# Performance work log

Measured on AMD Instinct MI355X. Metric: run time of the kernel, lower is better.

The kernel has to match this reference:

```python
import jax, jax.numpy as jnp
import numpy as np

H, W = 260, 346          # DAVIS346 sensor resolution
TEMP = 256.0             # time-decay temperature
B, T = 16, 4096          # batch, event sequence length
C = 2 * H + 2 * W        # pred channel dim = 1212


def setup_inputs() -> dict:
    key = jax.random.key(0)
    k1, k2, k3, k4, k5 = jax.random.split(key, 5)
    pred = jax.random.normal(k1, (B, T, C), dtype=jnp.float32)
    # target columns: [timestamp, y_index, x_index, polarity]
    t = jnp.sort(jax.random.uniform(k2, (B, T), minval=0.0, maxval=1.0e6), axis=1)
    y = jax.random.randint(k3, (B, T), 0, H)
    x = jax.random.randint(k4, (B, T), 0, W)
    p = jax.random.randint(k5, (B, T), 0, 2)
    target = jnp.stack([t,
                        y.astype(jnp.float32),
                        x.astype(jnp.float32),
                        p.astype(jnp.float32)], axis=-1)  # [B,T,4]
    return {"pred": pred, "target": target}


def _loss(pred, target):
    t = target[..., 0]                          # [B,T] timestamps
    y = target[..., 1].astype(jnp.int32)        # row indices
    x = target[..., 2].astype(jnp.int32)        # col indices
    p = target[..., 3]                          # polarity in {0,1}
    p_ = p[..., None]

    oh_y = jax.nn.one_hot(y, H, dtype=pred.dtype)   # [B,T,H]
    oh_x = jax.nn.one_hot(x, W, dtype=pred.dtype)   # [B,T,W]
    # scatter targets, concatenated in pred's channel layout [H0|H1|W0|W1]
    base = jnp.concatenate([oh_y * (1.0 - p_), oh_y * p_,
                            oh_x * (1.0 - p_), oh_x * p_], axis=-1)  # [B,T,C]

    # exponential time decay between consecutive events: d_i = exp(-(t_{i+1}-t_i)/TEMP)
    decay = jnp.exp(-(t[:, 1:] - t[:, :-1]) / TEMP)  # [B,T-1]

    # reverse recurrence: s_{T-1} = base_{T-1}; s_i = base_i + d_i * s_{i+1} for i = T-2..1;
    # s_0 = base_0 (torch loop stops before updating index 0)
    base_tm = jnp.swapaxes(base, 0, 1)               # [T,B,C] time-major
    decay_tm = jnp.swapaxes(decay, 0, 1)[..., None]  # [T-1,B,1]

    def step(carry, xd):
        b, d = xd
        s = b + d * carry
        return s, s

    _, ys = jax.lax.scan(step, base_tm[-1], (base_tm[:-1], decay_tm), reverse=True)
    s = jnp.concatenate([ys, base_tm[-1:]], axis=0)  # [T,B,C]
    s = s.at[0].set(base_tm[0])                      # index 0 never accumulated
    s = jnp.swapaxes(s, 0, 1)                        # [B,T,C]

    segs = [(0, H), (H, 2 * H), (2 * H, 2 * H + W), (2 * H + W, C)]
    losses = []
    for a, b in segs:
        logp = jax.nn.log_softmax(pred[..., a:b], axis=-1)
        soft = jax.nn.softmax(s[..., a:b], axis=-1)
        losses.append(-(soft * logp).sum(-1))        # soft-target CE, [B,T]
    lH0, lH1, lW0, lW1 = losses

    loss = ((lH0 + lW0) * (1.0 - p) + (lH1 + lW1) * p).mean()
    return loss


def reference(pred, target):
    return _loss(pred, target)
```

## Files before the change

kernel.cpp:

```cpp
#include <hip/hip_runtime.h>

#define HH 260
#define WW 346
#define CC 1212
#define CP 1280
#define HALF 640
#define NA 606
#define BB 16
#define TT 4096
#define INV_TEMP (1.0f/256.0f)
#define KCH 256
#define LCH 16
#define NG 16
#define GSZ 16
#define GLEN (GSZ * LCH)
#define NJ 10

__global__ __launch_bounds__(256) void p1_local(const float* __restrict__ target,
                                                float* __restrict__ Lbuf) {
    const int blk = blockIdx.x;
    const int b = blk >> 6;
    const int k0 = (blk & 63) << 2;
    const int tid = threadIdx.x;
    const int w = tid >> 6, lane = tid & 63;
    const int k = k0 + w;
    const int a = k * LCH;

    __shared__ float tg[4][LCH][4];
    __shared__ float tnextS[4];
    tg[tid >> 6][(tid >> 2) & 15][tid & 3] =
        target[((size_t)b * TT + k0 * LCH) * 4 + tid];
    if (tid < 4) {
        const int kk = k0 + tid;
        tnextS[tid] = (kk < KCH - 1) ? target[((size_t)b * TT + (kk + 1) * LCH) * 4] : 0.0f;
    }
    __syncthreads();

    float s0[NJ], s1[NJ];
#pragma unroll
    for (int j = 0; j < NJ; ++j) { s0[j] = 0.f; s1[j] = 0.f; }

    for (int li = LCH - 1; li >= 0; --li) {
        const int i = a + li;
        const float ti = tg[w][li][0];
        const float tn = (li == LCH - 1) ? tnextS[w] : tg[w][li + 1][0];
        const float d = (i >= TT - 1) ? 0.0f : __expf(-(tn - ti) * INV_TEMP);
        const int y = (int)tg[w][li][1], x = (int)tg[w][li][2], p = (int)tg[w][li][3];
        const int uy = y, ux = 260 + x;
        if (p == 0) {
#pragma unroll
            for (int j = 0; j < NJ; ++j) {
                const int u = lane + 64 * j;
                const float add = (u == uy ? 1.f : 0.f) + (u == ux ? 1.f : 0.f);
                s0[j] = fmaf(s0[j], d, add);
                s1[j] *= d;
            }
        } else {
#pragma unroll
            for (int j = 0; j < NJ; ++j) {
                const int u = lane + 64 * j;
                const float add = (u == uy ? 1.f : 0.f) + (u == ux ? 1.f : 0.f);
                s1[j] = fmaf(s1[j], d, add);
                s0[j] *= d;
            }
        }
    }
    float* __restrict__ out = Lbuf + (size_t)(b * KCH + k) * CP;
#pragma unroll
    for (int j = 0; j < NJ; ++j) {
        out[lane + 64 * j] = s0[j];
        out[HALF + lane + 64 * j] = s1[j];
    }
}

__global__ __launch_bounds__(256) void p2a(const float* __restrict__ target,
                                           const float* __restrict__ Lbuf,
                                           float* __restrict__ LCin,
                                           float* __restrict__ GroupL) {
    const int blk = blockIdx.x;
    const int ct = blk % 5;
    const int bg = blk / 5;
    const int b = bg >> 4, g = bg & 15;
    const int c = ct * 256 + threadIdx.x;

    float carry = 0.f;
#pragma unroll
    for (int kk = GSZ - 1; kk >= 0; --kk) {
        const int k = g * GSZ + kk;
        const size_t idx = ((size_t)(b * KCH + k)) * CP + c;
        LCin[idx] = carry;
        float P = 0.f;
        if (k < KCH - 1) {
            const float ta = target[((size_t)b * TT + k * LCH) * 4];
            const float te = target[((size_t)b * TT + (k + 1) * LCH) * 4];
            P = __expf(-(te - ta) * INV_TEMP);
        }
        carry = fmaf(P, carry, Lbuf[idx]);
    }
    GroupL[(size_t)bg * CP + c] = carry;
}

__global__ __launch_bounds__(256) void p2b(const float* __restrict__ target,
                                           const float* __restrict__ GroupL,
                                           float* __restrict__ SC) {
    const int blk = blockIdx.x;
    const int ct = blk % 5;
    const int b = blk / 5;
    const int c = ct * 256 + threadIdx.x;

    float Gv[NG], GP[NG];
#pragma unroll
    for (int g = 0; g < NG; ++g)
        Gv[g] = GroupL[((size_t)(b * NG + g)) * CP + c];
#pragma unroll
    for (int g = 0; g < NG; ++g) {
        if (g < NG - 1) {
            const float ta = target[((size_t)b * TT + g * GLEN) * 4];
            const float te = target[((size_t)b * TT + (g + 1) * GLEN) * 4];
            GP[g] = __expf(-(te - ta) * INV_TEMP);
        } else GP[g] = 0.f;
    }
    float carry = 0.f;
#pragma unroll
    for (int g = NG - 1; g >= 0; --g) {
        SC[((size_t)(b * NG + g)) * CP + c] = carry;
        carry = fmaf(GP[g], carry, Gv[g]);
    }
}

__global__ __launch_bounds__(256, 6) void p3_loss(const float* __restrict__ pred,
                                                  const float* __restrict__ target,
                                                  const float* __restrict__ LCin,
                                                  const float* __restrict__ SC,
                                                  double* __restrict__ partials) {
    const int blk = blockIdx.x;
    const int b = blk >> 6;
    const int k0 = (blk & 63) << 2;
    const int tid = threadIdx.x;
    const int w = tid >> 6, lane = tid & 63;
    const int k = k0 + w;
    const int g = k >> 4;
    const int a = k * LCH;

    __shared__ float tg[4][LCH][4];
    __shared__ float tnextS[4];
    tg[tid >> 6][(tid >> 2) & 15][tid & 3] =
        target[((size_t)b * TT + k0 * LCH) * 4 + tid];
    if (tid < 4) {
        const int kk = k0 + tid;
        tnextS[tid] = (kk < KCH - 1) ? target[((size_t)b * TT + (kk + 1) * LCH) * 4] : 0.0f;
    }
    __syncthreads();

    float Qk = 0.f;
    if (g < NG - 1) {
        const float tge = target[((size_t)b * TT + (g + 1) * GLEN) * 4];
        const float tk1 = target[((size_t)b * TT + (k + 1) * LCH) * 4];
        Qk = __expf(-(tge - tk1) * INV_TEMP);
    }

    const float* __restrict__ lc = LCin + (size_t)(b * KCH + k) * CP;
    const float* __restrict__ sc = SC + ((size_t)(b * NG + g)) * CP;
    float s0[NJ], s1[NJ];
#pragma unroll
    for (int j = 0; j < NJ; ++j) {
        const int u = lane + 64 * j;
        s0[j] = fmaf(Qk, sc[u], lc[u]);
        s1[j] = fmaf(Qk, sc[HALF + u], lc[HALF + u]);
    }

    float prA[NJ], prB[NJ];
    {
        const int p = (int)tg[w][LCH - 1][3];
        const float* __restrict__ prow = pred + ((size_t)b * TT + a + LCH - 1) * CC;
#pragma unroll
        for (int j = 0; j < NJ; ++j) {
            const int u = lane + 64 * j;
            const int c = (u < 260) ? p * HH + u : 2 * HH + p * WW + (u - 260);
            prA[j] = (u < NA) ? prow[c] : 0.0f;
        }
    }

    double lacc = 0.0;
    for (int li = LCH - 1; li >= 0; --li) {
        if (li > 0) {
            const int pn = (int)tg[w][li - 1][3];
            const float* __restrict__ prow = pred + ((size_t)b * TT + a + li - 1) * CC;
#pragma unroll
            for (int j = 0; j < NJ; ++j) {
                const int u = lane + 64 * j;
                const int c = (u < 260) ? pn * HH + u : 2 * HH + pn * WW + (u - 260);
                prB[j] = (u < NA) ? prow[c] : 0.0f;
            }
        }

        const int i = a + li;
        const float ti = tg[w][li][0];
        const float tn = (li == LCH - 1) ? tnextS[w] : tg[w][li + 1][0];
        const float d = (i == 0 || i >= TT - 1) ? 0.0f : __expf(-(tn - ti) * INV_TEMP);
        const int y = (int)tg[w][li][1], x = (int)tg[w][li][2], p = (int)tg[w][li][3];
        const int uy = y, ux = 260 + x;

        float zpy = 0.f, zsy = 0.f, dty = 0.f;
        float zpx = 0.f, zsx = 0.f, dtx = 0.f;

        auto stepActive = [&](float (&SA)[NJ], float (&SO)[NJ]) {
#pragma unroll
            for (int j = 0; j < NJ; ++j) {
                const int u = lane + 64 * j;
                const float add = (u == uy ? 1.f : 0.f) + (u == ux ? 1.f : 0.f);
                SA[j] = fmaf(SA[j], d, add);
                SO[j] *= d;
                float es = __expf(SA[j]);
                float ep = __expf(prA[j]);
                if (j == NJ - 1) {
                    const float m = (u < NA) ? 1.f : 0.f;
                    es *= m; ep *= m;
                }
                if (j < 4) {
                    zpy += ep; zsy += es; dty = fmaf(es, prA[j], dty);
                } else if (j == 4) {
                    const bool isY = (u < 260);
                    zpy += isY ? ep : 0.f;
                    zsy += isY ? es : 0.f;
                    dty = fmaf(isY ? es : 0.f, prA[j], dty);
                    zpx += isY ? 0.f : ep;
                    zsx += isY ? 0.f : es;
                    dtx = fmaf(isY ? 0.f : es, prA[j], dtx);
                } else {
                    zpx += ep; zsx += es; dtx = fmaf(es, prA[j], dtx);
                }
            }
        };
        if (p == 0) stepActive(s0, s1); else stepActive(s1, s0);

#pragma unroll
        for (int off = 32; off > 0; off >>= 1) {
            zpy += __shfl_xor(zpy, off);
            zsy += __shfl_xor(zsy, off);
            dty += __shfl_xor(dty, off);
            zpx += __shfl_xor(zpx, off);
            zsx += __shfl_xor(zsx, off);
            dtx += __shfl_xor(dtx, off);
        }
        const float loss = __logf(zpy) + __logf(zpx)
                         - __fdividef(dty, zsy) - __fdividef(dtx, zsx);
        lacc += (double)loss;

#pragma unroll
        for (int j = 0; j < NJ; ++j) prA[j] = prB[j];
    }
    if (lane == 0) partials[b * KCH + k] = lacc;
}

__global__ void p4_final(const double* __restrict__ partials, float* __restrict__ out) {
    const int tid = threadIdx.x;
    double sum = 0.0;
    for (int i = tid; i < BB * KCH; i += 256) sum += partials[i];
#pragma unroll
    for (int off = 32; off > 0; off >>= 1) sum += __shfl_xor(sum, off);
    __shared__ double sred[4];
    if ((tid & 63) == 0) sred[tid >> 6] = sum;
    __syncthreads();
    if (tid == 0)
        out[0] = (float)((sred[0] + sred[1] + sred[2] + sred[3]) / (double)((size_t)BB * TT));
}

extern "C" void kernel_launch(void* const* d_in, const int* in_sizes, int n_in,
                              void* d_out, int out_size, void* d_ws, size_t ws_size,
                              hipStream_t stream) {
    const float* pred   = (const float*)d_in[0];
    const float* target = (const float*)d_in[1];
    float* out = (float*)d_out;

    double* partials = (double*)d_ws;
    float* Lbuf   = (float*)((char*)d_ws + 65536);
    float* LCin   = Lbuf + (size_t)BB * KCH * CP;
    float* GroupL = LCin + (size_t)BB * KCH * CP;
    float* SC     = GroupL + (size_t)BB * NG * CP;

    p1_local<<<BB * KCH / 4, 256, 0, stream>>>(target, Lbuf);
    p2a<<<BB * NG * 5, 256, 0, stream>>>(target, Lbuf, LCin, GroupL);
    p2b<<<BB * 5, 256, 0, stream>>>(target, GroupL, SC);
    p3_loss<<<BB * KCH / 4, 256, 0, stream>>>(pred, target, LCin, SC, partials);
    p4_final<<<1, 256, 0, stream>>>(partials, out);
}
```

Baseline: 82.13 us.

## Fuse local and group scan kernels, vectorize loss loads with double-buffered rows

Merges the per-chunk local scan and the group carry scan into one kernel that keeps events in shared memory and scans sequentially per channel. This removes the Lbuf intermediate write and read. The loss kernel moves to an interleaved float2 channel layout for vectorized loads of LCin, SC and pred rows, and double-buffers two pred rows to hide latency. The occupancy hint drops from 6 to 4 blocks per CU to allow more registers. The fused scan does 256 serial steps per thread, which lengthens its critical path.

New measurement: 96.51 us. 17.5% more time.

```diff
diff --git a/kernel.cpp b/kernel.cpp
--- a/kernel.cpp
+++ b/kernel.cpp
@@ -14,88 +14,41 @@
 #define NG 16
 #define GSZ 16
 #define GLEN (GSZ * LCH)
-#define NJ 10
-
-__global__ __launch_bounds__(256) void p1_local(const float* __restrict__ target,
-                                                float* __restrict__ Lbuf) {
+
+__global__ __launch_bounds__(256) void p12_scan(const float* __restrict__ target,
+                                                float* __restrict__ LCin,
+                                                float* __restrict__ GroupL) {
     const int blk = blockIdx.x;
-    const int b = blk >> 6;
-    const int k0 = (blk & 63) << 2;
-    const int tid = threadIdx.x;
-    const int w = tid >> 6, lane = tid & 63;
-    const int k = k0 + w;
-    const int a = k * LCH;
-
-    __shared__ float tg[4][LCH][4];
-    __shared__ float tnextS[4];
-    tg[tid >> 6][(tid >> 2) & 15][tid & 3] =
-        target[((size_t)b * TT + k0 * LCH) * 4 + tid];
-    if (tid < 4) {
-        const int kk = k0 + tid;
-        tnextS[tid] = (kk < KCH - 1) ? target[((size_t)b * TT + (kk + 1) * LCH) * 4] : 0.0f;
-    }
-    __syncthreads();
-
-    float s0[NJ], s1[NJ];
-#pragma unroll
-    for (int j = 0; j < NJ; ++j) { s0[j] = 0.f; s1[j] = 0.f; }
-
-    for (int li = LCH - 1; li >= 0; --li) {
-        const int i = a + li;
-        const float ti = tg[w][li][0];
-        const float tn = (li == LCH - 1) ? tnextS[w] : tg[w][li + 1][0];
-        const float d = (i >= TT - 1) ? 0.0f : __expf(-(tn - ti) * INV_TEMP);
-        const int y = (int)tg[w][li][1], x = (int)tg[w][li][2], p = (int)tg[w][li][3];
-        const int uy = y, ux = 260 + x;
-        if (p == 0) {
-#pragma unroll
-            for (int j = 0; j < NJ; ++j) {
-                const int u = lane + 64 * j;
-                const float add = (u == uy ? 1.f : 0.f) + (u == ux ? 1.f : 0.f);
-                s0[j] = fmaf(s0[j], d, add);
-                s1[j] *= d;
-            }
-        } else {
-#pragma unroll
-            for (int j = 0; j < NJ; ++j) {
-                const int u = lane + 64 * j;
-                const float add = (u == uy ? 1.f : 0.f) + (u == ux ? 1.f : 0.f);
-                s1[j] = fmaf(s1[j], d, add);
-                s0[j] *= d;
-            }
-        }
-    }
-    float* __restrict__ out = Lbuf + (size_t)(b * KCH + k) * CP;
-#pragma unroll
-    for (int j = 0; j < NJ; ++j) {
-        out[lane + 64 * j] = s0[j];
-        out[HALF + lane + 64 * j] = s1[j];
-    }
-}
-
-__global__ __launch_bounds__(256) void p2a(const float* __restrict__ target,
-                                           const float* __restrict__ Lbuf,
-                                           float* __restrict__ LCin,
-                                           float* __restrict__ GroupL) {
-    const int blk = blockIdx.x;
-    const int ct = blk % 5;
+    const int sl = blk % 5;
     const int bg = blk / 5;
     const int b = bg >> 4, g = bg & 15;
-    const int c = ct * 256 + threadIdx.x;
+    const int tid = threadIdx.x;
+    const int c = sl * 256 + tid;
+    const int a0 = g * GLEN;
+
+    __shared__ float tg[GLEN][4];
+    __shared__ float tnextS;
+    for (int idx = tid; idx < GLEN * 4; idx += 256)
+        tg[idx >> 2][idx & 3] = target[((size_t)b * TT + a0) * 4 + idx];
+    if (tid == 0) tnextS = (a0 + GLEN < TT) ? target[((size_t)b * TT + a0 + GLEN) * 4] : 0.0f;
+    __syncthreads();
 
     float carry = 0.f;
-#pragma unroll
-    for (int kk = GSZ - 1; kk >= 0; --kk) {
-        const int k = g * GSZ + kk;
-        const size_t idx = ((size_t)(b * KCH + k)) * CP + c;
-        LCin[idx] = carry;
-        float P = 0.f;
-        if (k < KCH - 1) {
-            const float ta = target[((size_t)b * TT + k * LCH) * 4];
-            const float te = target[((size_t)b * TT + (k + 1) * LCH) * 4];
-            P = __expf(-(te - ta) * INV_TEMP);
+    for (int k = GSZ - 1; k >= 0; --k) {
+        LCin[((size_t)(b * KCH + g * GSZ + k)) * CP + c] = carry;
+#pragma unroll
+        for (int q = LCH - 1; q >= 0; --q) {
+            const int li = k * LCH + q;
+            const int i = a0 + li;
+            const float ti = tg[li][0];
+            const float tn = (li == GLEN - 1) ? tnextS : tg[li + 1][0];
+            const float d = (i >= TT - 1) ? 0.f : __expf(-(tn - ti) * INV_TEMP);
+            const int y = (int)tg[li][1], x = (int)tg[li][2], p = (int)tg[li][3];
+            const int cy = p * HALF + y;
+            const int cx = p * HALF + 260 + x;
+            const float add = ((c == cy) ? 1.f : 0.f) + ((c == cx) ? 1.f : 0.f);
+            carry = fmaf(carry, d, add);
         }
-        carry = fmaf(P, carry, Lbuf[idx]);
     }
     GroupL[(size_t)bg * CP + c] = carry;
 }
@@ -128,7 +81,7 @@
     }
 }
 
-__global__ __launch_bounds__(256, 6) void p3_loss(const float* __restrict__ pred,
+__global__ __launch_bounds__(256, 4) void p3_loss(const float* __restrict__ pred,
                                                   const float* __restrict__ target,
                                                   const float* __restrict__ LCin,
                                                   const float* __restrict__ SC,
@@ -161,39 +114,41 @@
 
     const float* __restrict__ lc = LCin + (size_t)(b * KCH + k) * CP;
     const float* __restrict__ sc = SC + ((size_t)(b * NG + g)) * CP;
-    float s0[NJ], s1[NJ];
-#pragma unroll
-    for (int j = 0; j < NJ; ++j) {
-        const int u = lane + 64 * j;
-        s0[j] = fmaf(Qk, sc[u], lc[u]);
-        s1[j] = fmaf(Qk, sc[HALF + u], lc[HALF + u]);
-    }
-
-    float prA[NJ], prB[NJ];
-    {
-        const int p = (int)tg[w][LCH - 1][3];
-        const float* __restrict__ prow = pred + ((size_t)b * TT + a + LCH - 1) * CC;
-#pragma unroll
-        for (int j = 0; j < NJ; ++j) {
-            const int u = lane + 64 * j;
-            const int c = (u < 260) ? p * HH + u : 2 * HH + p * WW + (u - 260);
-            prA[j] = (u < NA) ? prow[c] : 0.0f;
+    float s0[10], s1[10];
+#pragma unroll
+    for (int q = 0; q < 5; ++q) {
+        const int u0 = (q * 64 + lane) * 2;
+        const float2 l0 = *(const float2*)(lc + u0);
+        const float2 c0 = *(const float2*)(sc + u0);
+        const float2 l1 = *(const float2*)(lc + HALF + u0);
+        const float2 c1 = *(const float2*)(sc + HALF + u0);
+        s0[2 * q]     = fmaf(Qk, c0.x, l0.x);
+        s0[2 * q + 1] = fmaf(Qk, c0.y, l0.y);
+        s1[2 * q]     = fmaf(Qk, c1.x, l1.x);
+        s1[2 * q + 1] = fmaf(Qk, c1.y, l1.y);
+    }
+
+    auto loadRow = [&](float (&pr)[10], int li) {
+        const int pn = (int)tg[w][li][3];
+        const float* __restrict__ prow = pred + ((size_t)b * TT + a + li) * CC;
+#pragma unroll
+        for (int q = 0; q < 5; ++q) {
+            const int u0 = (q * 64 + lane) * 2;
+            float2 v;
+            if (u0 < 260) {
+                v = *(const float2*)(prow + pn * HH + u0);
+            } else if (u0 < NA) {
+                v = *(const float2*)(prow + 2 * HH + pn * WW + (u0 - 260));
+            } else {
+                v = make_float2(0.f, 0.f);
+            }
+            pr[2 * q] = v.x; pr[2 * q + 1] = v.y;
         }
-    }
+    };
 
     double lacc = 0.0;
-    for (int li = LCH - 1; li >= 0; --li) {
-        if (li > 0) {
-            const int pn = (int)tg[w][li - 1][3];
-            const float* __restrict__ prow = pred + ((size_t)b * TT + a + li - 1) * CC;
-#pragma unroll
-            for (int j = 0; j < NJ; ++j) {
-                const int u = lane + 64 * j;
-                const int c = (u < 260) ? pn * HH + u : 2 * HH + pn * WW + (u - 260);
-                prB[j] = (u < NA) ? prow[c] : 0.0f;
-            }
-        }
-
+
+    auto step = [&](int li, float (&pr)[10]) {
         const int i = a + li;
         const float ti = tg[w][li][0];
         const float tn = (li == LCH - 1) ? tnextS[w] : tg[w][li + 1][0];
@@ -204,35 +159,31 @@
         float zpy = 0.f, zsy = 0.f, dty = 0.f;
         float zpx = 0.f, zsx = 0.f, dtx = 0.f;
 
-        auto stepActive = [&](float (&SA)[NJ], float (&SO)[NJ]) {
-#pragma unroll
-            for (int j = 0; j < NJ; ++j) {
-                const int u = lane + 64 * j;
-                const float add = (u == uy ? 1.f : 0.f) + (u == ux ? 1.f : 0.f);
-                SA[j] = fmaf(SA[j], d, add);
-                SO[j] *= d;
-                float es = __expf(SA[j]);
-                float ep = __expf(prA[j]);
-                if (j == NJ - 1) {
-                    const float m = (u < NA) ? 1.f : 0.f;
-                    es *= m; ep *= m;
-                }
-                if (j < 4) {
-                    zpy += ep; zsy += es; dty = fmaf(es, prA[j], dty);
-                } else if (j == 4) {
-                    const bool isY = (u < 260);
-                    zpy += isY ? ep : 0.f;
-                    zsy += isY ? es : 0.f;
-                    dty = fmaf(isY ? es : 0.f, prA[j], dty);
-                    zpx += isY ? 0.f : ep;
-                    zsx += isY ? 0.f : es;
-                    dtx = fmaf(isY ? 0.f : es, prA[j], dtx);
-                } else {
-                    zpx += ep; zsx += es; dtx = fmaf(es, prA[j], dtx);
+        auto inner = [&](float (&SA)[10], float (&SO)[10]) {
+#pragma unroll
+            for (int q = 0; q < 5; ++q) {
+#pragma unroll
+                for (int e = 0; e < 2; ++e) {
+                    const int j = 2 * q + e;
+                    const int u = (q * 64 + lane) * 2 + e;
+                    const float add = ((u == uy) ? 1.f : 0.f) + ((u == ux) ? 1.f : 0.f);
+                    SA[j] = fmaf(SA[j], d, add);
+                    SO[j] *= d;
+                    float es = __expf(SA[j]);
+                    float ep = __expf(pr[j]);
+                    if (q == 4) {
+                        const float m = (u < NA) ? 1.f : 0.f;
+                        es *= m; ep *= m;
+                    }
+                    if (u < 260) {
+                        zpy += ep; zsy += es; dty = fmaf(es, pr[j], dty);
+                    } else {
+                        zpx += ep; zsx += es; dtx = fmaf(es, pr[j], dtx);
+                    }
                 }
             }
         };
-        if (p == 0) stepActive(s0, s1); else stepActive(s1, s0);
+        if (p == 0) inner(s0, s1); else inner(s1, s0);
 
 #pragma unroll
         for (int off = 32; off > 0; off >>= 1) {
@@ -246,10 +197,20 @@
         const float loss = __logf(zpy) + __logf(zpx)
                          - __fdividef(dty, zsy) - __fdividef(dtx, zsx);
         lacc += (double)loss;
-
-#pragma unroll
-        for (int j = 0; j < NJ; ++j) prA[j] = prB[j];
-    }
+    };
+
+    float prA[10], prB[10];
+    loadRow(prA, LCH - 1);
+    loadRow(prB, LCH - 2);
+    for (int t = 0; t < LCH / 2; ++t) {
+        const int liA = LCH - 1 - 2 * t;
+        step(liA, prA);
+        if (liA - 2 >= 0) loadRow(prA, liA - 2);
+        const int liB = LCH - 2 - 2 * t;
+        step(liB, prB);
+        if (liB - 2 >= 0) loadRow(prB, liB - 2);
+    }
+
     if (lane == 0) partials[b * KCH + k] = lacc;
 }
 
@@ -274,13 +235,11 @@
     float* out = (float*)d_out;
 
     double* partials = (double*)d_ws;
-    float* Lbuf   = (float*)((char*)d_ws + 65536);
-    float* LCin   = Lbuf + (size_t)BB * KCH * CP;
+    float* LCin   = (float*)((char*)d_ws + 65536);
     float* GroupL = LCin + (size_t)BB * KCH * CP;
     float* SC     = GroupL + (size_t)BB * NG * CP;
 
-    p1_local<<<BB * KCH / 4, 256, 0, stream>>>(target, Lbuf);
-    p2a<<<BB * NG * 5, 256, 0, stream>>>(target, Lbuf, LCin, GroupL);
+    p12_scan<<<BB * NG * 5, 256, 0, stream>>>(target, LCin, GroupL);
     p2b<<<BB * 5, 256, 0, stream>>>(target, GroupL, SC);
     p3_loss<<<BB * KCH / 4, 256, 0, stream>>>(pred, target, LCin, SC, partials);
     p4_final<<<1, 256, 0, stream>>>(partials, out);
```

## Stage pred rows via async global-to-LDS loads with double buffering in loss kernel

Applied to the files above, without the earlier changes.

The loss kernel now prefetches each pred row with global_load_lds straight into a per-wave double buffer in shared memory and waits on vmcnt, replacing the previous register prefetch. It also makes the per-event scalars wave-uniform with readfirstlane and replaces the per-element one-hot compare with a row/lane test. Blocks shrink to 128 threads (2 waves) with twice as many blocks. The aim is to cut register pressure and overlap memory latency with the exp-heavy compute, at the cost of relying on hand-written waitcnt counts being correct.

Result: slower. 86.86 us (+5.8%).

```diff
diff --git a/kernel.cpp b/kernel.cpp
--- a/kernel.cpp
+++ b/kernel.cpp
@@ -16,6 +16,10 @@
 #define GLEN (GSZ * LCH)
 #define NJ 10
 
+#define GLDS(gsrc, ldst) __builtin_amdgcn_global_load_lds( \
+    (const __attribute__((address_space(1))) void*)(gsrc), \
+    (__attribute__((address_space(3))) void*)(ldst), 4, 0, 0)
+
 __global__ __launch_bounds__(256) void p1_local(const float* __restrict__ target,
                                                 float* __restrict__ Lbuf) {
     const int blk = blockIdx.x;
@@ -128,28 +132,28 @@
     }
 }
 
-__global__ __launch_bounds__(256, 6) void p3_loss(const float* __restrict__ pred,
+__global__ __launch_bounds__(128, 4) void p3_loss(const float* __restrict__ pred,
                                                   const float* __restrict__ target,
                                                   const float* __restrict__ LCin,
                                                   const float* __restrict__ SC,
                                                   double* __restrict__ partials) {
     const int blk = blockIdx.x;
-    const int b = blk >> 6;
-    const int k0 = (blk & 63) << 2;
+    const int b = blk >> 7;
+    const int kp = (blk & 127) << 1;
     const int tid = threadIdx.x;
     const int w = tid >> 6, lane = tid & 63;
-    const int k = k0 + w;
+    const int k = kp + w;
     const int g = k >> 4;
     const int a = k * LCH;
 
-    __shared__ float tg[4][LCH][4];
-    __shared__ float tnextS[4];
+    __shared__ float tg[2][LCH][4];
+    __shared__ float tnextS[2];
+    __shared__ float pbuf[2][2][HALF];
+
     tg[tid >> 6][(tid >> 2) & 15][tid & 3] =
-        target[((size_t)b * TT + k0 * LCH) * 4 + tid];
-    if (tid < 4) {
-        const int kk = k0 + tid;
-        tnextS[tid] = (kk < KCH - 1) ? target[((size_t)b * TT + (kk + 1) * LCH) * 4] : 0.0f;
-    }
+        target[((size_t)b * TT + kp * LCH) * 4 + tid];
+    if (lane == 0)
+        tnextS[w] = (k < KCH - 1) ? target[((size_t)b * TT + (k + 1) * LCH) * 4] : 0.0f;
     __syncthreads();
 
     float Qk = 0.f;
@@ -169,70 +173,76 @@
         s1[j] = fmaf(Qk, sc[HALF + u], lc[HALF + u]);
     }
 
-    float prA[NJ], prB[NJ];
-    {
-        const int p = (int)tg[w][LCH - 1][3];
-        const float* __restrict__ prow = pred + ((size_t)b * TT + a + LCH - 1) * CC;
+    auto stage = [&](int li, int buf) {
+        const int pn = __builtin_amdgcn_readfirstlane((int)tg[w][li][3]);
+        const float* prow = pred + ((size_t)b * TT + a + li) * CC;
+        const float* pY = prow + pn * HH;
+        const float* pX = prow + 260 + pn * WW;
+        float* lb = &pbuf[w][buf][0];
 #pragma unroll
         for (int j = 0; j < NJ; ++j) {
             const int u = lane + 64 * j;
-            const int c = (u < 260) ? p * HH + u : 2 * HH + p * WW + (u - 260);
-            prA[j] = (u < NA) ? prow[c] : 0.0f;
+            const float* gsrc;
+            if (j <= 3)      gsrc = pY + u;
+            else if (j == 4) gsrc = (u < 260) ? (pY + u) : (pX + u);
+            else if (j <= 8) gsrc = pX + u;
+            else             gsrc = (u < NA) ? (pX + u) : prow;
+            GLDS(gsrc, lb + 64 * j);
         }
-    }
+    };
 
     double lacc = 0.0;
-    for (int li = LCH - 1; li >= 0; --li) {
-        if (li > 0) {
-            const int pn = (int)tg[w][li - 1][3];
-            const float* __restrict__ prow = pred + ((size_t)b * TT + a + li - 1) * CC;
-#pragma unroll
-            for (int j = 0; j < NJ; ++j) {
-                const int u = lane + 64 * j;
-                const int c = (u < 260) ? pn * HH + u : 2 * HH + pn * WW + (u - 260);
-                prB[j] = (u < NA) ? prow[c] : 0.0f;
-            }
-        }
-
+
+    auto step = [&](int li, int buf) {
         const int i = a + li;
         const float ti = tg[w][li][0];
         const float tn = (li == LCH - 1) ? tnextS[w] : tg[w][li + 1][0];
-        const float d = (i == 0 || i >= TT - 1) ? 0.0f : __expf(-(tn - ti) * INV_TEMP);
-        const int y = (int)tg[w][li][1], x = (int)tg[w][li][2], p = (int)tg[w][li][3];
-        const int uy = y, ux = 260 + x;
+        float d = (i == 0 || i >= TT - 1) ? 0.0f : __expf(-(tn - ti) * INV_TEMP);
+        d = __int_as_float(__builtin_amdgcn_readfirstlane(__float_as_int(d)));
+        const int uy = __builtin_amdgcn_readfirstlane((int)tg[w][li][1]);
+        const int ux = 260 + __builtin_amdgcn_readfirstlane((int)tg[w][li][2]);
+        const int pS = __builtin_amdgcn_readfirstlane((int)tg[w][li][3]);
+        const int ry = uy >> 6, ly = uy & 63;
+        const int rx = ux >> 6, lx = ux & 63;
+        const float vy = (lane == ly) ? 1.f : 0.f;
+        const float vx = (lane == lx) ? 1.f : 0.f;
+        const float* lb = &pbuf[w][buf][0];
 
         float zpy = 0.f, zsy = 0.f, dty = 0.f;
         float zpx = 0.f, zsx = 0.f, dtx = 0.f;
 
-        auto stepActive = [&](float (&SA)[NJ], float (&SO)[NJ]) {
+        auto inner = [&](float (&SA)[NJ], float (&SO)[NJ]) {
 #pragma unroll
             for (int j = 0; j < NJ; ++j) {
                 const int u = lane + 64 * j;
-                const float add = (u == uy ? 1.f : 0.f) + (u == ux ? 1.f : 0.f);
-                SA[j] = fmaf(SA[j], d, add);
+                float sv = SA[j] * d;
+                if (ry == j) sv += vy;
+                if (rx == j) sv += vx;
+                SA[j] = sv;
                 SO[j] *= d;
-                float es = __expf(SA[j]);
-                float ep = __expf(prA[j]);
+                const float pr = lb[64 * j + lane];
+                float es = __expf(sv);
+                float ep = __expf(pr);
                 if (j == NJ - 1) {
                     const float m = (u < NA) ? 1.f : 0.f;
                     es *= m; ep *= m;
                 }
                 if (j < 4) {
-                    zpy += ep; zsy += es; dty = fmaf(es, prA[j], dty);
+                    zpy += ep; zsy += es; dty = fmaf(es, pr, dty);
                 } else if (j == 4) {
                     const bool isY = (u < 260);
                     zpy += isY ? ep : 0.f;
                     zsy += isY ? es : 0.f;
-                    dty = fmaf(isY ? es : 0.f, prA[j], dty);
+                    dty = fmaf(isY ? es : 0.f, pr, dty);
                     zpx += isY ? 0.f : ep;
                     zsx += isY ? 0.f : es;
-                    dtx = fmaf(isY ? 0.f : es, prA[j], dtx);
+                    dtx = fmaf(isY ? 0.f : es, pr, dtx);
                 } else {
-                    zpx += ep; zsx += es; dtx = fmaf(es, prA[j], dtx);
+                    zpx += ep; zsx += es; dtx = fmaf(es, pr, dtx);
                 }
             }
         };
-        if (p == 0) stepActive(s0, s1); else stepActive(s1, s0);
+        if (pS == 0) inner(s0, s1); else inner(s1, s0);
 
 #pragma unroll
         for (int off = 32; off > 0; off >>= 1) {
@@ -246,10 +256,19 @@
         const float loss = __logf(zpy) + __logf(zpx)
                          - __fdividef(dty, zsy) - __fdividef(dtx, zsx);
         lacc += (double)loss;
-
-#pragma unroll
-        for (int j = 0; j < NJ; ++j) prA[j] = prB[j];
-    }
+    };
+
+    stage(LCH - 1, 0);
+    int cur = 0;
+    for (int li = LCH - 1; li >= 1; --li) {
+        stage(li - 1, cur ^ 1);
+        asm volatile("s_waitcnt vmcnt(10)" ::: "memory");
+        step(li, cur);
+        cur ^= 1;
+    }
+    asm volatile("s_waitcnt vmcnt(0)" ::: "memory");
+    step(0, cur);
+
     if (lane == 0) partials[b * KCH + k] = lacc;
 }
 
@@ -282,6 +301,6 @@
     p1_local<<<BB * KCH / 4, 256, 0, stream>>>(target, Lbuf);
     p2a<<<BB * NG * 5, 256, 0, stream>>>(target, Lbuf, LCin, GroupL);
     p2b<<<BB * 5, 256, 0, stream>>>(target, GroupL, SC);
-    p3_loss<<<BB * KCH / 4, 256, 0, stream>>>(pred, target, LCin, SC, partials);
+    p3_loss<<<BB * KCH / 2, 128, 0, stream>>>(pred, target, LCin, SC, partials);
     p4_final<<<1, 256, 0, stream>>>(partials, out);
 }
```

## Split loss kernel into separate H and W segment blocks to double parallelism

Applied to the files above, without the earlier changes.

The loss kernel now launches a second grid dimension so the H segment (260 wide) and the W segment (346 wide) are handled by separate blocks, each keeping 5 or 6 register columns per plane instead of 10. This halves the per-wave serial work and register footprint, and the launch bound is raised to 8 waves per SIMD for more occupancy. The trade-off is that target metadata, the time decays and the per-row exponentials are recomputed in both blocks. The partials buffer also doubles in size, and the final reduction sums both halves.

Result: slower. 124.9 us (+52.1%).

```diff
diff --git a/kernel.cpp b/kernel.cpp
--- a/kernel.cpp
+++ b/kernel.cpp
@@ -128,12 +128,17 @@
     }
 }
 
-__global__ __launch_bounds__(256, 6) void p3_loss(const float* __restrict__ pred,
-                                                  const float* __restrict__ target,
-                                                  const float* __restrict__ LCin,
-                                                  const float* __restrict__ SC,
-                                                  double* __restrict__ partials) {
-    const int blk = blockIdx.x;
+template <int SEG>
+__device__ __forceinline__ void p3_seg(const float* __restrict__ pred,
+                                       const float* __restrict__ target,
+                                       const float* __restrict__ LCin,
+                                       const float* __restrict__ SC,
+                                       double* __restrict__ partials,
+                                       int blk) {
+    constexpr int NR = (SEG == 0) ? 5 : 6;
+    constexpr int SEGLEN = (SEG == 0) ? HH : WW;
+    constexpr int SOFF = (SEG == 0) ? 0 : 260;
+
     const int b = blk >> 6;
     const int k0 = (blk & 63) << 2;
     const int tid = threadIdx.x;
@@ -159,104 +164,96 @@
         Qk = __expf(-(tge - tk1) * INV_TEMP);
     }
 
-    const float* __restrict__ lc = LCin + (size_t)(b * KCH + k) * CP;
-    const float* __restrict__ sc = SC + ((size_t)(b * NG + g)) * CP;
-    float s0[NJ], s1[NJ];
-#pragma unroll
-    for (int j = 0; j < NJ; ++j) {
-        const int u = lane + 64 * j;
-        s0[j] = fmaf(Qk, sc[u], lc[u]);
-        s1[j] = fmaf(Qk, sc[HALF + u], lc[HALF + u]);
-    }
-
-    float prA[NJ], prB[NJ];
-    {
-        const int p = (int)tg[w][LCH - 1][3];
-        const float* __restrict__ prow = pred + ((size_t)b * TT + a + LCH - 1) * CC;
-#pragma unroll
-        for (int j = 0; j < NJ; ++j) {
+    const float* __restrict__ lc = LCin + (size_t)(b * KCH + k) * CP + SOFF;
+    const float* __restrict__ sc = SC + ((size_t)(b * NG + g)) * CP + SOFF;
+    float sA[2][NR];
+#pragma unroll
+    for (int pl = 0; pl < 2; ++pl)
+#pragma unroll
+        for (int j = 0; j < NR; ++j) {
             const int u = lane + 64 * j;
-            const int c = (u < 260) ? p * HH + u : 2 * HH + p * WW + (u - 260);
-            prA[j] = (u < NA) ? prow[c] : 0.0f;
-        }
-    }
+            const int uc = (u < SEGLEN) ? u : (SEGLEN - 1);
+            const float v = fmaf(Qk, sc[pl * HALF + uc], lc[pl * HALF + uc]);
+            sA[pl][j] = (u < SEGLEN) ? v : 0.f;
+        }
+
+    auto loadRow = [&](float (&pr)[NR], int li) {
+        const int pn = (int)tg[w][li][3];
+        const float* __restrict__ prow = pred + ((size_t)b * TT + a + li) * CC
+                                       + (SEG == 0 ? pn * HH : 2 * HH + pn * WW);
+#pragma unroll
+        for (int j = 0; j < NR; ++j) {
+            const int u = lane + 64 * j;
+            pr[j] = prow[(u < SEGLEN) ? u : (SEGLEN - 1)];
+        }
+    };
 
     double lacc = 0.0;
-    for (int li = LCH - 1; li >= 0; --li) {
-        if (li > 0) {
-            const int pn = (int)tg[w][li - 1][3];
-            const float* __restrict__ prow = pred + ((size_t)b * TT + a + li - 1) * CC;
-#pragma unroll
-            for (int j = 0; j < NJ; ++j) {
-                const int u = lane + 64 * j;
-                const int c = (u < 260) ? pn * HH + u : 2 * HH + pn * WW + (u - 260);
-                prB[j] = (u < NA) ? prow[c] : 0.0f;
-            }
-        }
-
+
+    auto step = [&](int li, float (&pr)[NR]) {
         const int i = a + li;
         const float ti = tg[w][li][0];
         const float tn = (li == LCH - 1) ? tnextS[w] : tg[w][li + 1][0];
         const float d = (i == 0 || i >= TT - 1) ? 0.0f : __expf(-(tn - ti) * INV_TEMP);
-        const int y = (int)tg[w][li][1], x = (int)tg[w][li][2], p = (int)tg[w][li][3];
-        const int uy = y, ux = 260 + x;
-
-        float zpy = 0.f, zsy = 0.f, dty = 0.f;
-        float zpx = 0.f, zsx = 0.f, dtx = 0.f;
-
-        auto stepActive = [&](float (&SA)[NJ], float (&SO)[NJ]) {
-#pragma unroll
-            for (int j = 0; j < NJ; ++j) {
+        const int ev = (int)tg[w][li][SEG == 0 ? 1 : 2];
+        const int p = (int)tg[w][li][3];
+
+        float zp = 0.f, zs = 0.f, dt = 0.f;
+
+        auto inner = [&](float (&SA)[NR], float (&SO)[NR]) {
+#pragma unroll
+            for (int j = 0; j < NR; ++j) {
                 const int u = lane + 64 * j;
-                const float add = (u == uy ? 1.f : 0.f) + (u == ux ? 1.f : 0.f);
+                const float add = (u == ev) ? 1.f : 0.f;
                 SA[j] = fmaf(SA[j], d, add);
                 SO[j] *= d;
+                const float prv = pr[j];
                 float es = __expf(SA[j]);
-                float ep = __expf(prA[j]);
-                if (j == NJ - 1) {
-                    const float m = (u < NA) ? 1.f : 0.f;
+                float ep = __expf(prv);
+                if (j == NR - 1) {
+                    const float m = (u < SEGLEN) ? 1.f : 0.f;
                     es *= m; ep *= m;
                 }
-                if (j < 4) {
-                    zpy += ep; zsy += es; dty = fmaf(es, prA[j], dty);
-                } else if (j == 4) {
-                    const bool isY = (u < 260);
-                    zpy += isY ? ep : 0.f;
-                    zsy += isY ? es : 0.f;
-                    dty = fmaf(isY ? es : 0.f, prA[j], dty);
-                    zpx += isY ? 0.f : ep;
-                    zsx += isY ? 0.f : es;
-                    dtx = fmaf(isY ? 0.f : es, prA[j], dtx);
-                } else {
-                    zpx += ep; zsx += es; dtx = fmaf(es, prA[j], dtx);
-                }
+                zp += ep; zs += es; dt = fmaf(es, prv, dt);
             }
         };
-        if (p == 0) stepActive(s0, s1); else stepActive(s1, s0);
+        if (p == 0) inner(sA[0], sA[1]); else inner(sA[1], sA[0]);
 
 #pragma unroll
         for (int off = 32; off > 0; off >>= 1) {
-            zpy += __shfl_xor(zpy, off);
-            zsy += __shfl_xor(zsy, off);
-            dty += __shfl_xor(dty, off);
-            zpx += __shfl_xor(zpx, off);
-            zsx += __shfl_xor(zsx, off);
-            dtx += __shfl_xor(dtx, off);
-        }
-        const float loss = __logf(zpy) + __logf(zpx)
-                         - __fdividef(dty, zsy) - __fdividef(dtx, zsx);
-        lacc += (double)loss;
-
-#pragma unroll
-        for (int j = 0; j < NJ; ++j) prA[j] = prB[j];
-    }
-    if (lane == 0) partials[b * KCH + k] = lacc;
+            zp += __shfl_xor(zp, off);
+            zs += __shfl_xor(zs, off);
+            dt += __shfl_xor(dt, off);
+        }
+        lacc += (double)(__logf(zp) - __fdividef(dt, zs));
+    };
+
+    float prA[NR], prB[NR];
+    loadRow(prA, LCH - 1);
+    for (int li = LCH - 1; li >= 1; --li) {
+        loadRow(prB, li - 1);
+        step(li, prA);
+#pragma unroll
+        for (int j = 0; j < NR; ++j) prA[j] = prB[j];
+    }
+    step(0, prA);
+
+    if (lane == 0) partials[SEG * (BB * KCH) + b * KCH + k] = lacc;
+}
+
+__global__ __launch_bounds__(256, 8) void p3_loss(const float* __restrict__ pred,
+                                                  const float* __restrict__ target,
+                                                  const float* __restrict__ LCin,
+                                                  const float* __restrict__ SC,
+                                                  double* __restrict__ partials) {
+    if (blockIdx.y == 0) p3_seg<0>(pred, target, LCin, SC, partials, blockIdx.x);
+    else                 p3_seg<1>(pred, target, LCin, SC, partials, blockIdx.x);
 }
 
 __global__ void p4_final(const double* __restrict__ partials, float* __restrict__ out) {
     const int tid = threadIdx.x;
     double sum = 0.0;
-    for (int i = tid; i < BB * KCH; i += 256) sum += partials[i];
+    for (int i = tid; i < 2 * BB * KCH; i += 256) sum += partials[i];
 #pragma unroll
     for (int off = 32; off > 0; off >>= 1) sum += __shfl_xor(sum, off);
     __shared__ double sred[4];
@@ -282,6 +279,7 @@
     p1_local<<<BB * KCH / 4, 256, 0, stream>>>(target, Lbuf);
     p2a<<<BB * NG * 5, 256, 0, stream>>>(target, Lbuf, LCin, GroupL);
     p2b<<<BB * 5, 256, 0, stream>>>(target, GroupL, SC);
-    p3_loss<<<BB * KCH / 4, 256, 0, stream>>>(pred, target, LCin, SC, partials);
+    dim3 g3(BB * KCH / 4, 2);
+    p3_loss<<<g3, 256, 0, stream>>>(pred, target, LCin, SC, partials);
     p4_final<<<1, 256, 0, stream>>>(partials, out);
 }
```
